# Kernel optimization log

Measured on AMD Instinct MI355X. Metric: run time of the kernel, lower is better.

The kernel has to match this reference:

```python
import jax, jax.numpy as jnp
import numpy as np

K = 5            # neighborhood kernel size
PAD = 2
CENTER = (K * K) // 2   # index 12: the pixel itself
TEMP = 0.1       # InfoNCE temperature
EPS = 1e-8
NUM_CLASSES = 2


def _patches_f(x):
    """x: [B,H,W,C] float -> [B,H,W,K*K,C] zero-padded 5x5 neighborhoods."""
    B, H, W, C = x.shape
    xp = jnp.pad(x, ((0, 0), (PAD, PAD), (PAD, PAD), (0, 0)))
    return jnp.stack([xp[:, i:i + H, j:j + W, :]
                      for i in range(K) for j in range(K)], axis=3)


def _patches_i(x):
    """x: [B,H,W] int -> [B,H,W,K*K] zero-padded 5x5 neighborhoods."""
    B, H, W = x.shape
    xp = jnp.pad(x, ((0, 0), (PAD, PAD), (PAD, PAD)))
    return jnp.stack([xp[:, i:i + H, j:j + W]
                      for i in range(K) for j in range(K)], axis=3)


def setup_inputs() -> dict:
    key = jax.random.key(0)
    k1, k2, k3, k4 = jax.random.split(key, 4)
    B, C, H, W = 2, 256, 96, 96
    return {
        "er_input": jax.random.normal(k1, (B, C, H, W), dtype=jnp.float32),
        "seg_logit": jax.random.normal(k2, (B, NUM_CLASSES, H, W), dtype=jnp.float32),
        "seg_label": jax.random.randint(k3, (B, H, W), 0, NUM_CLASSES, dtype=jnp.int32),
        "gt_boundary_seg": jax.random.randint(k4, (B, H, W), 0, 2, dtype=jnp.int32),
    }


def reference(er_input, seg_logit, seg_label, gt_boundary_seg):
    # er_input: [B,C,H,W]; seg_logit: [B,nc,H,W]; labels: [B,H,W]
    feat = er_input.transpose(0, 2, 3, 1)          # [B,H,W,C]
    pred = jnp.argmax(seg_logit, axis=1)           # [B,H,W]
    gt_b = jnp.where(gt_boundary_seg == 255, 0, gt_boundary_seg)
    edge = gt_b.astype(bool)                       # boundary mask [B,H,W]

    neigh_feat = _patches_f(feat)                  # [B,H,W,25,C]
    neigh_label = _patches_i(seg_label)            # [B,H,W,25]
    neigh_pred = _patches_i(pred)                  # [B,H,W,25]

    def correct(c):
        # one_hot(label)*one_hot(pred) at class c, per neighbor
        return ((neigh_label == c) & (neigh_pred == c)).astype(feat.dtype)

    a_norm_neigh = jnp.linalg.norm(neigh_feat, axis=-1)   # [B,H,W,25]

    total = jnp.asarray(0.0, dtype=feat.dtype)
    shown = list(range(NUM_CLASSES))               # shown_class (both assumed present)
    n_cls = len(shown)
    for i in range(n_cls):
        c = shown[i]
        c_pre = shown[(i - 1) % n_cls]
        c_post = shown[(i + 1) % n_cls]

        now_mask = (seg_label == c)                # [B,H,W]
        neigh_is_c = (neigh_label == c).astype(feat.dtype)
        # same-class neighbor count, center excluded (kernel has 0 at center)
        count = neigh_is_c.sum(-1) - neigh_is_c[..., CENTER]
        pix_mask = ((count >= 1) & edge & now_mask).astype(feat.dtype)  # [B,H,W]

        w_now = correct(c)                         # [B,H,W,25]
        w_neg = correct(c_pre) + correct(c_post)   # pre_class + post_class weights

        # anchor = center feature * correct indicator (taken before zeroing center)
        anchor = neigh_feat[..., CENTER, :] * w_now[..., CENTER, None]  # [B,H,W,C]
        # positive = mean over 25 neighbors of (feat * correct), center zeroed
        positive = (jnp.einsum('bhwkc,bhwk->bhwc', neigh_feat, w_now) - anchor) / (K * K)

        a_norm = jnp.linalg.norm(anchor, axis=-1)  # [B,H,W]
        p_norm = jnp.linalg.norm(positive, axis=-1)
        pos_cos = (anchor * positive).sum(-1) / (a_norm * p_norm + EPS)   # [B,H,W]

        # negatives: per-offset features weighted by (pre+post) correctness
        dots = jnp.einsum('bhwc,bhwkc->bhwk', anchor, neigh_feat)         # [B,H,W,25]
        neg_cos = (dots * w_neg) / (a_norm[..., None] * a_norm_neigh * w_neg + EPS)

        logits = jnp.concatenate([pos_cos[..., None], neg_cos], axis=-1) / TEMP
        loss_pix = -jax.nn.log_softmax(logits, axis=-1)[..., 0]          # [B,H,W]

        total = total + (loss_pix * pix_mask).sum() / jnp.maximum(pix_mask.sum(), 1.0)
    return total
```

## Files before the change

kernel.cpp:

```cpp
#include <hip/hip_runtime.h>
#include <math.h>

#define Hc 96
#define Wc 96
#define Bc 2
#define Cc 256
#define HWc (Hc * Wc)
#define NKc 25
#define NPIX (Bc * HWc)
#define NSLOT 32

#define OFF_ACC 0
#define OFF_CNT (NSLOT * 2 * 4)
#define OFF_MIS (OFF_CNT + 8)
#define OFF_HC (OFF_MIS + 8)
#define HDR_FLOATS 80
#define OFF_NRM2 320
#define OFF_PRED (OFF_NRM2 + NPIX * 4)
#define OFF_WL (OFF_PRED + NPIX * 4)
#define OFF_FT (OFF_WL + NPIX * 16)

__device__ __forceinline__ float wave_reduce_sum(float v) {
#pragma unroll
  for (int off = 32; off > 0; off >>= 1) v += __shfl_xor(v, off);
  return v;
}

__global__ __launch_bounds__(256) void transpose_kernel(
    const float* __restrict__ in, const float* __restrict__ seg_logit,
    float* __restrict__ out, float* __restrict__ nrm2, int* __restrict__ pred,
    float* __restrict__ hdr) {
  __shared__ float tile[32][33];
  __shared__ float part[8][32];
  const int bx = blockIdx.x;
  const int b = blockIdx.y;
  const int tx = threadIdx.x;
  const int ty = threadIdx.y;
  const float* src = in + (size_t)b * Cc * HWc;
  float* dst = out + (size_t)b * HWc * Cc;
  const int p0 = bx * 32;

  if (bx == 0 && b == 0) {
    const int t = ty * 32 + tx;
    if (t < HDR_FLOATS) hdr[t] = 0.f;
  }

  float psum = 0.f;
  for (int by = 0; by < 8; ++by) {
    const int c0 = by * 32;
#pragma unroll
    for (int i = 0; i < 4; i++)
      tile[ty + i * 8][tx] = src[(size_t)(c0 + ty + i * 8) * HWc + p0 + tx];
    __syncthreads();
#pragma unroll
    for (int i = 0; i < 4; i++)
      dst[(size_t)(p0 + ty + i * 8) * Cc + c0 + tx] = tile[tx][ty + i * 8];
#pragma unroll
    for (int i = 0; i < 4; i++) {
      const float v = tile[ty * 4 + i][tx];
      psum += v * v;
    }
    __syncthreads();
  }
  part[ty][tx] = psum;
  __syncthreads();
  if (ty == 0) {
    float t = 0.f;
#pragma unroll
    for (int j = 0; j < 8; j++) t += part[j][tx];
    const int hw = p0 + tx;
    nrm2[b * HWc + hw] = t;
    const float l0 = seg_logit[(size_t)(b * 2 + 0) * HWc + hw];
    const float l1 = seg_logit[(size_t)(b * 2 + 1) * HWc + hw];
    pred[b * HWc + hw] = (l1 > l0) ? 1 : 0;
  }
}

__global__ __launch_bounds__(256) void classify_kernel(
    const int* __restrict__ label, const int* __restrict__ gtb,
    const int* __restrict__ pred, const float* __restrict__ nrm2,
    float* __restrict__ cnt, float* __restrict__ mis,
    unsigned int* __restrict__ heavyCount, uint4* __restrict__ worklist) {
  __shared__ unsigned int s_cnt[4];
  if (threadIdx.x < 4) s_cnt[threadIdx.x] = 0;
  __syncthreads();
  const int tid = blockIdx.x * 256 + threadIdx.x;
  bool heavy = false;
  int c = 0;
  unsigned mNow = 0, mNeg = 0;
  float a_norm = 0.f;
  {
    const int hw = tid % HWc;
    const int h = hw / Wc, w = hw % Wc;
    int g = gtb[tid];
    if (g == 255) g = 0;
    if (g) {
      c = label[tid];
      const int oc = 1 - c;
      const int pc = pred[tid];
      int count = 0;
#pragma unroll
      for (int k = 0; k < NKc; k++) {
        const int di = k / 5 - 2, dj = k % 5 - 2;
        const int hh = h + di, ww = w + dj;
        const bool inb = (hh >= 0) && (hh < Hc) && (ww >= 0) && (ww < Wc);
        int lb = 0, pr = 0;
        if (inb) {
          const int n = tid + di * Wc + dj;
          lb = label[n];
          pr = pred[n];
        }
        count += (lb == c);
        if (inb) {
          if (lb == c && pr == c) mNow |= 1u << k;
          if (lb == oc && pr == oc) mNeg |= 1u << k;
        }
      }
      count -= 1;
      if (count >= 1) {
        atomicAdd(&s_cnt[c], 1u);
        if (pc == c) {
          heavy = true;
          a_norm = sqrtf(nrm2[tid]);
        } else {
          atomicAdd(&s_cnt[2 + c], 1u);
        }
      }
    }
  }
  const unsigned long long m = __ballot(heavy);
  const int lane = threadIdx.x & 63;
  if (m) {
    unsigned int base = 0;
    if (lane == 0) base = atomicAdd(heavyCount, (unsigned)__popcll(m));
    base = __shfl(base, 0);
    if (heavy) {
      const unsigned idx = base + (unsigned)__popcll(m & ((1ull << lane) - 1ull));
      worklist[idx] = make_uint4((unsigned)tid | ((unsigned)c << 16), mNow, mNeg,
                                 __float_as_uint(a_norm));
    }
  }
  __syncthreads();
  if (threadIdx.x < 2) {
    if (s_cnt[threadIdx.x]) atomicAdd(&cnt[threadIdx.x], (float)s_cnt[threadIdx.x]);
    if (s_cnt[2 + threadIdx.x]) atomicAdd(&mis[threadIdx.x], (float)s_cnt[2 + threadIdx.x]);
  }
}

__global__ __launch_bounds__(256) void heavy_kernel(
    const float* __restrict__ featT, const float* __restrict__ nrm2,
    const unsigned int* __restrict__ heavyCount,
    const uint4* __restrict__ worklist, float* __restrict__ accum) {
  __shared__ float s_loss[2];
  if (threadIdx.x < 2) s_loss[threadIdx.x] = 0.f;
  __syncthreads();
  const int lane = threadIdx.x & 63;
  const int wv = threadIdx.x >> 6;
  const unsigned nH = *heavyCount;
  const unsigned nw = gridDim.x * 4;
  const float4* fp = (const float4*)featT;
  float lacc0 = 0.f, lacc1 = 0.f;
  for (unsigned i = blockIdx.x * 4 + wv; i < nH; i += nw) {
    const uint4 e = worklist[i];
    const int wid = e.x & 0xffff;
    const int c = (e.x >> 16) & 1;
    const unsigned mNow = e.y, mNeg = e.z;
    const float a_norm = __uint_as_float(e.w);

    float nkv = 0.f;
    if (lane < NKc && ((mNeg >> lane) & 1u))
      nkv = sqrtf(nrm2[wid + (lane / 5 - 2) * Wc + (lane % 5 - 2)]);

    const float4 anchor = fp[(size_t)wid * 64 + lane];
    float4 pos = make_float4(0.f, 0.f, 0.f, 0.f);
    float dpart[NKc];
    const unsigned mAny = mNow | mNeg;
#pragma unroll
    for (int k = 0; k < NKc; k++) {
      dpart[k] = 0.f;
      if ((mAny >> k) & 1u) {
        const int off = wid + (k / 5 - 2) * Wc + (k % 5 - 2);
        const float4 f = fp[(size_t)off * 64 + lane];
        if ((mNow >> k) & 1u) {
          pos.x += f.x; pos.y += f.y; pos.z += f.z; pos.w += f.w;
        }
        if ((mNeg >> k) & 1u)
          dpart[k] = anchor.x * f.x + anchor.y * f.y + anchor.z * f.z + anchor.w * f.w;
      }
    }
    float4 pv;
    pv.x = (pos.x - anchor.x) * (1.0f / 25.0f);
    pv.y = (pos.y - anchor.y) * (1.0f / 25.0f);
    pv.z = (pos.z - anchor.z) * (1.0f / 25.0f);
    pv.w = (pos.w - anchor.w) * (1.0f / 25.0f);
    const float p2 = wave_reduce_sum(pv.x * pv.x + pv.y * pv.y + pv.z * pv.z + pv.w * pv.w);
    const float ad = wave_reduce_sum(anchor.x * pv.x + anchor.y * pv.y +
                                     anchor.z * pv.z + anchor.w * pv.w);
    const float x0 = (ad / (a_norm * sqrtf(p2) + 1e-8f)) * 10.0f;
    float mx = fmaxf(x0, 0.f);
#pragma unroll
    for (int k = 0; k < NKc; k++) {
      if ((mNeg >> k) & 1u) {
        const float d = wave_reduce_sum(dpart[k]);
        const float nk = __shfl(nkv, k);
        dpart[k] = ((d * 2.0f) / (a_norm * nk * 2.0f + 1e-8f)) * 10.0f;
        mx = fmaxf(mx, dpart[k]);
      }
    }
    float s = expf(x0 - mx) + (float)(NKc - __popc(mNeg)) * expf(-mx);
#pragma unroll
    for (int k = 0; k < NKc; k++)
      if ((mNeg >> k) & 1u) s += expf(dpart[k] - mx);
    const float loss = mx + logf(s) - x0;
    if (lane == 0) {
      if (c == 0) lacc0 += loss; else lacc1 += loss;
    }
  }
  if (lane == 0) {
    if (lacc0 != 0.f) atomicAdd(&s_loss[0], lacc0);
    if (lacc1 != 0.f) atomicAdd(&s_loss[1], lacc1);
  }
  __syncthreads();
  if (threadIdx.x < 2) {
    const float v = s_loss[threadIdx.x];
    if (v != 0.f) atomicAdd(&accum[(blockIdx.x & (NSLOT - 1)) * 2 + threadIdx.x], v);
  }
}

__global__ void finalize_kernel(const float* __restrict__ accum,
                                const float* __restrict__ cnt,
                                const float* __restrict__ mis,
                                float* __restrict__ out) {
  const int lane = threadIdx.x;
  float l0 = 0.f, l1 = 0.f;
  if (lane < NSLOT) {
    l0 = accum[lane * 2 + 0];
    l1 = accum[lane * 2 + 1];
  }
  l0 = wave_reduce_sum(l0);
  l1 = wave_reduce_sum(l1);
  if (lane == 0) {
    const float LOG26 = logf(26.0f);
    out[0] = (l0 + LOG26 * mis[0]) / fmaxf(cnt[0], 1.0f) +
             (l1 + LOG26 * mis[1]) / fmaxf(cnt[1], 1.0f);
  }
}

extern "C" void kernel_launch(void* const* d_in, const int* in_sizes, int n_in,
                              void* d_out, int out_size, void* d_ws, size_t ws_size,
                              hipStream_t stream) {
  const float* er = (const float*)d_in[0];
  const float* seg_logit = (const float*)d_in[1];
  const int* seg_label = (const int*)d_in[2];
  const int* gtb = (const int*)d_in[3];
  float* out = (float*)d_out;

  char* ws = (char*)d_ws;
  float* hdr = (float*)ws;
  float* accum = (float*)(ws + OFF_ACC);
  float* cnt = (float*)(ws + OFF_CNT);
  float* mis = (float*)(ws + OFF_MIS);
  unsigned int* heavyCount = (unsigned int*)(ws + OFF_HC);
  float* nrm2 = (float*)(ws + OFF_NRM2);
  int* pred = (int*)(ws + OFF_PRED);
  uint4* worklist = (uint4*)(ws + OFF_WL);
  float* featT = (float*)(ws + OFF_FT);

  dim3 tb(32, 8, 1);
  dim3 tg(HWc / 32, Bc, 1);
  transpose_kernel<<<tg, tb, 0, stream>>>(er, seg_logit, featT, nrm2, pred, hdr);

  classify_kernel<<<NPIX / 256, 256, 0, stream>>>(seg_label, gtb, pred, nrm2,
                                                  cnt, mis, heavyCount, worklist);

  heavy_kernel<<<1152, 256, 0, stream>>>(featT, nrm2, heavyCount, worklist, accum);

  finalize_kernel<<<1, 64, 0, stream>>>(accum, cnt, mis, out);
}
```

Measured before the change: 51.82 us.

## Pack label/pred into byte meta, make heavy loads branchless, fuse finalize via last-block

Label and prediction are packed into one byte per pixel during the transpose, so the classify kernel reads a single byte per neighbour instead of two ints. The heavy kernel now loads all 25 neighbours unconditionally, using clamped offsets and FMA weights in place of mask branches, and gives each block a contiguous chunk of the worklist for locality. The finalize kernel is removed: the last block to finish, found through a done counter, performs the final reduction. The unconditional loads add memory traffic for masked-out neighbours, and the fused finalize relies on the done counter being zeroed by the header clear.

```diff
diff --git a/kernel.cpp b/kernel.cpp
--- a/kernel.cpp
+++ b/kernel.cpp
@@ -11,13 +11,14 @@
 #define NSLOT 32
 
 #define OFF_ACC 0
-#define OFF_CNT (NSLOT * 2 * 4)
-#define OFF_MIS (OFF_CNT + 8)
-#define OFF_HC (OFF_MIS + 8)
+#define OFF_CNT 256
+#define OFF_MIS 264
+#define OFF_HC 272
+#define OFF_DONE 276
 #define HDR_FLOATS 80
 #define OFF_NRM2 320
-#define OFF_PRED (OFF_NRM2 + NPIX * 4)
-#define OFF_WL (OFF_PRED + NPIX * 4)
+#define OFF_META (OFF_NRM2 + NPIX * 4)
+#define OFF_WL (OFF_META + NPIX)
 #define OFF_FT (OFF_WL + NPIX * 16)
 
 __device__ __forceinline__ float wave_reduce_sum(float v) {
@@ -28,7 +29,8 @@
 
 __global__ __launch_bounds__(256) void transpose_kernel(
     const float* __restrict__ in, const float* __restrict__ seg_logit,
-    float* __restrict__ out, float* __restrict__ nrm2, int* __restrict__ pred,
+    const int* __restrict__ seg_label, float* __restrict__ out,
+    float* __restrict__ nrm2, unsigned char* __restrict__ meta,
     float* __restrict__ hdr) {
   __shared__ float tile[32][33];
   __shared__ float part[8][32];
@@ -69,18 +71,20 @@
 #pragma unroll
     for (int j = 0; j < 8; j++) t += part[j][tx];
     const int hw = p0 + tx;
-    nrm2[b * HWc + hw] = t;
+    const int gi = b * HWc + hw;
+    nrm2[gi] = t;
     const float l0 = seg_logit[(size_t)(b * 2 + 0) * HWc + hw];
     const float l1 = seg_logit[(size_t)(b * 2 + 1) * HWc + hw];
-    pred[b * HWc + hw] = (l1 > l0) ? 1 : 0;
+    const int pr = (l1 > l0) ? 1 : 0;
+    meta[gi] = (unsigned char)((seg_label[gi] & 1) | (pr << 1));
   }
 }
 
 __global__ __launch_bounds__(256) void classify_kernel(
-    const int* __restrict__ label, const int* __restrict__ gtb,
-    const int* __restrict__ pred, const float* __restrict__ nrm2,
-    float* __restrict__ cnt, float* __restrict__ mis,
-    unsigned int* __restrict__ heavyCount, uint4* __restrict__ worklist) {
+    const unsigned char* __restrict__ meta, const int* __restrict__ gtb,
+    const float* __restrict__ nrm2, float* __restrict__ cnt,
+    float* __restrict__ mis, unsigned int* __restrict__ heavyCount,
+    uint4* __restrict__ worklist) {
   __shared__ unsigned int s_cnt[4];
   if (threadIdx.x < 4) s_cnt[threadIdx.x] = 0;
   __syncthreads();
@@ -95,21 +99,18 @@
     int g = gtb[tid];
     if (g == 255) g = 0;
     if (g) {
-      c = label[tid];
+      const int m0 = meta[tid];
+      c = m0 & 1;
+      const int pc = (m0 >> 1) & 1;
       const int oc = 1 - c;
-      const int pc = pred[tid];
       int count = 0;
 #pragma unroll
       for (int k = 0; k < NKc; k++) {
         const int di = k / 5 - 2, dj = k % 5 - 2;
         const int hh = h + di, ww = w + dj;
         const bool inb = (hh >= 0) && (hh < Hc) && (ww >= 0) && (ww < Wc);
-        int lb = 0, pr = 0;
-        if (inb) {
-          const int n = tid + di * Wc + dj;
-          lb = label[n];
-          pr = pred[n];
-        }
+        const int mv = inb ? (int)meta[tid + di * Wc + dj] : 0;
+        const int lb = mv & 1, pr = (mv >> 1) & 1;
         count += (lb == c);
         if (inb) {
           if (lb == c && pr == c) mNow |= 1u << k;
@@ -150,17 +151,22 @@
 __global__ __launch_bounds__(256) void heavy_kernel(
     const float* __restrict__ featT, const float* __restrict__ nrm2,
     const unsigned int* __restrict__ heavyCount,
-    const uint4* __restrict__ worklist, float* __restrict__ accum) {
+    const uint4* __restrict__ worklist, float* __restrict__ accum,
+    unsigned int* __restrict__ doneCnt, const float* __restrict__ cnt,
+    const float* __restrict__ mis, float* __restrict__ out) {
   __shared__ float s_loss[2];
+  __shared__ unsigned s_last;
   if (threadIdx.x < 2) s_loss[threadIdx.x] = 0.f;
   __syncthreads();
   const int lane = threadIdx.x & 63;
   const int wv = threadIdx.x >> 6;
   const unsigned nH = *heavyCount;
-  const unsigned nw = gridDim.x * 4;
+  const unsigned chunk = (nH + gridDim.x - 1) / gridDim.x;
+  const unsigned lo = blockIdx.x * chunk;
+  const unsigned hi = min(lo + chunk, nH);
   const float4* fp = (const float4*)featT;
   float lacc0 = 0.f, lacc1 = 0.f;
-  for (unsigned i = blockIdx.x * 4 + wv; i < nH; i += nw) {
+  for (unsigned i = lo + wv; i < hi; i += 4) {
     const uint4 e = worklist[i];
     const int wid = e.x & 0xffff;
     const int c = (e.x >> 16) & 1;
@@ -174,19 +180,18 @@
     const float4 anchor = fp[(size_t)wid * 64 + lane];
     float4 pos = make_float4(0.f, 0.f, 0.f, 0.f);
     float dpart[NKc];
-    const unsigned mAny = mNow | mNeg;
 #pragma unroll
     for (int k = 0; k < NKc; k++) {
-      dpart[k] = 0.f;
-      if ((mAny >> k) & 1u) {
-        const int off = wid + (k / 5 - 2) * Wc + (k % 5 - 2);
-        const float4 f = fp[(size_t)off * 64 + lane];
-        if ((mNow >> k) & 1u) {
-          pos.x += f.x; pos.y += f.y; pos.z += f.z; pos.w += f.w;
-        }
-        if ((mNeg >> k) & 1u)
-          dpart[k] = anchor.x * f.x + anchor.y * f.y + anchor.z * f.z + anchor.w * f.w;
-      }
+      int off = wid + (k / 5 - 2) * Wc + (k % 5 - 2);
+      off = max(off, 0);
+      off = min(off, NPIX - 1);
+      const float4 f = fp[(size_t)off * 64 + lane];
+      const float wN = (float)((mNow >> k) & 1u);
+      pos.x = fmaf(f.x, wN, pos.x);
+      pos.y = fmaf(f.y, wN, pos.y);
+      pos.z = fmaf(f.z, wN, pos.z);
+      pos.w = fmaf(f.w, wN, pos.w);
+      dpart[k] = anchor.x * f.x + anchor.y * f.y + anchor.z * f.z + anchor.w * f.w;
     }
     float4 pv;
     pv.x = (pos.x - anchor.x) * (1.0f / 25.0f);
@@ -225,24 +230,22 @@
     const float v = s_loss[threadIdx.x];
     if (v != 0.f) atomicAdd(&accum[(blockIdx.x & (NSLOT - 1)) * 2 + threadIdx.x], v);
   }
-}
-
-__global__ void finalize_kernel(const float* __restrict__ accum,
-                                const float* __restrict__ cnt,
-                                const float* __restrict__ mis,
-                                float* __restrict__ out) {
-  const int lane = threadIdx.x;
-  float l0 = 0.f, l1 = 0.f;
-  if (lane < NSLOT) {
-    l0 = accum[lane * 2 + 0];
-    l1 = accum[lane * 2 + 1];
-  }
-  l0 = wave_reduce_sum(l0);
-  l1 = wave_reduce_sum(l1);
-  if (lane == 0) {
-    const float LOG26 = logf(26.0f);
-    out[0] = (l0 + LOG26 * mis[0]) / fmaxf(cnt[0], 1.0f) +
-             (l1 + LOG26 * mis[1]) / fmaxf(cnt[1], 1.0f);
+  __threadfence();
+  __syncthreads();
+  if (threadIdx.x == 0)
+    s_last = (atomicAdd(doneCnt, 1u) == (unsigned)(gridDim.x - 1)) ? 1u : 0u;
+  __syncthreads();
+  if (s_last && threadIdx.x < NSLOT * 2) {
+    const float v = atomicAdd(&accum[threadIdx.x], 0.0f);
+    float v0 = (threadIdx.x & 1) ? 0.f : v;
+    float v1 = (threadIdx.x & 1) ? v : 0.f;
+    v0 = wave_reduce_sum(v0);
+    v1 = wave_reduce_sum(v1);
+    if (threadIdx.x == 0) {
+      const float LOG26 = logf(26.0f);
+      out[0] = (v0 + LOG26 * mis[0]) / fmaxf(cnt[0], 1.0f) +
+               (v1 + LOG26 * mis[1]) / fmaxf(cnt[1], 1.0f);
+    }
   }
 }
 
@@ -261,19 +264,20 @@
   float* cnt = (float*)(ws + OFF_CNT);
   float* mis = (float*)(ws + OFF_MIS);
   unsigned int* heavyCount = (unsigned int*)(ws + OFF_HC);
+  unsigned int* doneCnt = (unsigned int*)(ws + OFF_DONE);
   float* nrm2 = (float*)(ws + OFF_NRM2);
-  int* pred = (int*)(ws + OFF_PRED);
+  unsigned char* meta = (unsigned char*)(ws + OFF_META);
   uint4* worklist = (uint4*)(ws + OFF_WL);
   float* featT = (float*)(ws + OFF_FT);
 
   dim3 tb(32, 8, 1);
   dim3 tg(HWc / 32, Bc, 1);
-  transpose_kernel<<<tg, tb, 0, stream>>>(er, seg_logit, featT, nrm2, pred, hdr);
-
-  classify_kernel<<<NPIX / 256, 256, 0, stream>>>(seg_label, gtb, pred, nrm2,
-                                                  cnt, mis, heavyCount, worklist);
-
-  heavy_kernel<<<1152, 256, 0, stream>>>(featT, nrm2, heavyCount, worklist, accum);
-
-  finalize_kernel<<<1, 64, 0, stream>>>(accum, cnt, mis, out);
-}
+  transpose_kernel<<<tg, tb, 0, stream>>>(er, seg_logit, seg_label, featT, nrm2,
+                                          meta, hdr);
+
+  classify_kernel<<<NPIX / 256, 256, 0, stream>>>(meta, gtb, nrm2, cnt, mis,
+                                                  heavyCount, worklist);
+
+  heavy_kernel<<<1152, 256, 0, stream>>>(featT, nrm2, heavyCount, worklist,
+                                         accum, doneCnt, cnt, mis, out);
+}
```

Measured after the change: 131.5 us. 154% more time.
